# Kernel optimization log

Hardware: AMD Instinct MI355X
Metric: run time of the kernel (lower is better)

## Reference

```python
import jax, jax.numpy as jnp
import numpy as np

C = 256
NH = 8
G = 32  # groupnorm groups (min(32, C))
EPS = 1e-6


def setup_inputs() -> dict:
    key = jax.random.key(0)
    ks = jax.random.split(key, 7)
    B, D, H, W = 2, 16, 16, 16
    x = jax.random.normal(ks[0], (B, C, D, H, W), dtype=jnp.float32)
    gn_gamma = jnp.ones((C,), jnp.float32)
    gn_beta = jnp.zeros((C,), jnp.float32)
    s = 1.0 / np.sqrt(C)
    qkv_w = jax.random.normal(ks[1], (3 * C, C), jnp.float32) * s  # 1x1x1 conv weight
    qkv_b = jnp.zeros((3 * C,), jnp.float32)
    proj_w = jax.random.normal(ks[2], (C, C), jnp.float32) * s
    proj_b = jnp.zeros((C,), jnp.float32)
    return {"x": x, "gn_gamma": gn_gamma, "gn_beta": gn_beta,
            "qkv_w": qkv_w, "qkv_b": qkv_b, "proj_w": proj_w, "proj_b": proj_b}


def _group_norm(x, gamma, beta):
    # x: [B, C, S]
    B, Cc, S = x.shape
    xg = x.reshape(B, G, (Cc // G) * S)
    mu = xg.mean(axis=-1, keepdims=True)
    var = xg.var(axis=-1, keepdims=True)
    xg = (xg - mu) * jax.lax.rsqrt(var + EPS)
    x = xg.reshape(B, Cc, S)
    return x * gamma[None, :, None] + beta[None, :, None]


def reference(x, gn_gamma, gn_beta, qkv_w, qkv_b, proj_w, proj_b):
    B, Cc, D, H, W = x.shape
    S = D * H * W
    hd = Cc // NH
    xf = x.reshape(B, Cc, S)
    h = _group_norm(xf, gn_gamma, gn_beta)
    # 1x1x1 conv == channel matmul: [B, 3C, S]
    qkv = jnp.einsum('oc,bcs->bos', qkv_w, h) + qkv_b[None, :, None]
    # torch path: reshape(B,3C,S).permute(0,2,1).chunk -> q=channels[0:C]
    q, k, v = qkv[:, :Cc], qkv[:, Cc:2 * Cc], qkv[:, 2 * Cc:]
    # [B, C, S] -> [B, NH, S, hd]
    def to_heads(t):
        return t.reshape(B, NH, hd, S).transpose(0, 1, 3, 2)
    q, k, v = to_heads(q), to_heads(k), to_heads(v)
    scale = hd ** (-0.5)
    attn = jax.nn.softmax(jnp.einsum('bnqd,bnkd->bnqk', q, k) * scale, axis=-1)
    o = jnp.einsum('bnqk,bnkd->bnqd', attn, v)  # [B, NH, S, hd]
    o = o.transpose(0, 1, 3, 2).reshape(B, Cc, S)  # back to [B, C, S]
    o = jnp.einsum('oc,bcs->bos', proj_w, o) + proj_b[None, :, None]
    return x + o.reshape(B, Cc, D, H, W)
```

## Files before the change

### kernel.cpp

```cpp
#include <hip/hip_runtime.h>
#include <cstddef>

#define S_LEN 4096
#define C_DIM 256
#define NHEADS 8
#define HDIM 32

typedef __attribute__((ext_vector_type(8))) _Float16 half8;
typedef __attribute__((ext_vector_type(4))) _Float16 half4;
typedef __attribute__((ext_vector_type(2))) _Float16 h2t;
typedef __attribute__((ext_vector_type(2))) __fp16 fp16x2;
typedef __attribute__((ext_vector_type(4))) float floatx4;

#define SC2F ((float)(0.17677669529663687 * 1.4426950408889634))

__global__ __launch_bounds__(256) void prep_stats(
    const float* __restrict__ qkv_w, const float* __restrict__ proj_w,
    const float* __restrict__ qkv_b, const float* __restrict__ x,
    _Float16* __restrict__ wq, _Float16* __restrict__ wp,
    float* __restrict__ qbias, float* __restrict__ pstat)
{
  const int blk = blockIdx.x;
  const int tid = threadIdx.x;
  if (blk < 512) {
    __shared__ float red[2][4];
    const int gb = blk >> 3, e = blk & 7;
    const int g = gb & 31, b = gb >> 5;
    const float* xb = x + ((size_t)b * C_DIM + g * 8) * S_LEN + e * 4096;
    const float4* x4 = (const float4*)xb;
    float sum = 0.f, sumsq = 0.f;
    #pragma unroll
    for (int i = 0; i < 4; ++i) {
      float4 v = x4[tid + i * 256];
      sum += v.x + v.y + v.z + v.w;
      sumsq += v.x * v.x + v.y * v.y + v.z * v.z + v.w * v.w;
    }
    for (int off = 1; off < 64; off <<= 1) {
      sum += __shfl_xor(sum, off, 64);
      sumsq += __shfl_xor(sumsq, off, 64);
    }
    const int wv = tid >> 6, lane = tid & 63;
    if (lane == 0) { red[0][wv] = sum; red[1][wv] = sumsq; }
    __syncthreads();
    if (tid == 0) {
      pstat[(gb * 8 + e) * 2 + 0] = red[0][0] + red[0][1] + red[0][2] + red[0][3];
      pstat[(gb * 8 + e) * 2 + 1] = red[1][0] + red[1][1] + red[1][2] + red[1][3];
    }
  } else {
    int idx = (blk - 512) * 256 + tid;
    if (idx < 768 * 256) {
      float v = qkv_w[idx];
      if (idx < 256 * 256) v *= SC2F;
      wq[idx] = (_Float16)v;
    } else if (idx < 768 * 256 + 256 * 256) {
      int i = idx - 768 * 256;
      wp[i] = (_Float16)proj_w[i];
    } else if (idx < 768 * 256 + 256 * 256 + 768) {
      int i = idx - (768 * 256 + 256 * 256);
      float bv = qkv_b[i];
      if (i < 256) bv *= SC2F;
      qbias[i] = bv;
    }
  }
}

__global__ __launch_bounds__(256) void xnorm(
    const float* __restrict__ x, const float* __restrict__ gamma,
    const float* __restrict__ beta, const float* __restrict__ pstat,
    _Float16* __restrict__ xt)
{
  __shared__ _Float16 Lt[16][264];
  const int tid = threadIdx.x;
  const int b = blockIdx.y;
  const int s0 = blockIdx.x * 16;
  const int c = tid;
  const int gb = b * 32 + (c >> 3);
  float s = 0.f, sq = 0.f;
  #pragma unroll
  for (int e = 0; e < 8; ++e) {
    s  += pstat[(gb * 8 + e) * 2 + 0];
    sq += pstat[(gb * 8 + e) * 2 + 1];
  }
  const float mean = s * (1.f / 32768.f);
  const float rstd = rsqrtf(sq * (1.f / 32768.f) - mean * mean + 1e-6f);
  const float ga = gamma[c] * rstd, be = beta[c] - mean * ga;
  const float4* xa = (const float4*)(x + ((size_t)b * C_DIM + c) * S_LEN + s0);
  #pragma unroll
  for (int i = 0; i < 4; ++i) {
    float4 v = xa[i];
    Lt[i * 4 + 0][c] = (_Float16)(v.x * ga + be);
    Lt[i * 4 + 1][c] = (_Float16)(v.y * ga + be);
    Lt[i * 4 + 2][c] = (_Float16)(v.z * ga + be);
    Lt[i * 4 + 3][c] = (_Float16)(v.w * ga + be);
  }
  __syncthreads();
  const int sl = tid >> 4, cc = (tid & 15) * 16;
  _Float16* dst = xt + ((size_t)b * S_LEN + s0 + sl) * C_DIM + cc;
  const _Float16* src = &Lt[sl][cc];
  *(half8*)(dst + 0) = *(const half8*)(src + 0);
  *(half8*)(dst + 8) = *(const half8*)(src + 8);
}

__global__ __launch_bounds__(256) void qkv_gemm(
    const _Float16* __restrict__ W, const float* __restrict__ bias,
    const _Float16* __restrict__ xt,
    _Float16* __restrict__ qo, _Float16* __restrict__ ko_,
    _Float16* __restrict__ vo)
{
  __shared__ __align__(16) _Float16 Ld[256 * 72];
  const int tid = threadIdx.x;
  const int b = blockIdx.z;
  const int s0 = blockIdx.y * 64;

  {
    const int sl = tid >> 2, cc = (tid & 3) * 64;
    const _Float16* src = xt + ((size_t)b * S_LEN + s0 + sl) * C_DIM + cc;
    _Float16* dst = &Ld[sl * 264 + cc];
    #pragma unroll
    for (int j = 0; j < 8; ++j)
      *(half8*)(dst + j * 8) = *(const half8*)(src + j * 8);
  }
  __syncthreads();

  const int lane = tid & 63, wv = tid >> 6;
  const int m = lane & 15, quad = lane >> 4;
  const int mtb = blockIdx.x * 16 + wv * 4;
  const _Float16* wrow[4];
  #pragma unroll
  for (int j = 0; j < 4; ++j)
    wrow[j] = W + (size_t)((mtb + j) * 16 + m) * C_DIM + quad * 8;
  const _Float16* lp = &Ld[m * 264 + quad * 8];

  floatx4 acc[4][4];
  #pragma unroll
  for (int j = 0; j < 4; ++j)
    #pragma unroll
    for (int s = 0; s < 4; ++s) acc[j][s] = (floatx4){0.f,0.f,0.f,0.f};

  #pragma unroll 2
  for (int k0 = 0; k0 < C_DIM; k0 += 32) {
    half8 b0 = *(const half8*)(lp + k0);
    half8 b1 = *(const half8*)(lp + 16 * 264 + k0);
    half8 b2 = *(const half8*)(lp + 32 * 264 + k0);
    half8 b3 = *(const half8*)(lp + 48 * 264 + k0);
    #pragma unroll
    for (int j = 0; j < 4; ++j) {
      half8 a = *(const half8*)(wrow[j] + k0);
      acc[j][0] = __builtin_amdgcn_mfma_f32_16x16x32_f16(a, b0, acc[j][0], 0, 0, 0);
      acc[j][1] = __builtin_amdgcn_mfma_f32_16x16x32_f16(a, b1, acc[j][1], 0, 0, 0);
      acc[j][2] = __builtin_amdgcn_mfma_f32_16x16x32_f16(a, b2, acc[j][2], 0, 0, 0);
      acc[j][3] = __builtin_amdgcn_mfma_f32_16x16x32_f16(a, b3, acc[j][3], 0, 0, 0);
    }
  }

  if (blockIdx.x < 2) {
    #pragma unroll
    for (int j = 0; j < 4; ++j) {
      const int ob = (mtb + j) * 16 + quad * 4;
      const float bv0 = bias[ob], bv1 = bias[ob + 1],
                  bv2 = bias[ob + 2], bv3 = bias[ob + 3];
      _Float16* dst = (ob < 256) ? qo : ko_;
      const int oo = ob & 255, n = oo >> 5, d0 = oo & 31;
      #pragma unroll
      for (int sub = 0; sub < 4; ++sub) {
        int s = s0 + sub * 16 + m;
        half4 h = { (_Float16)(acc[j][sub][0] + bv0), (_Float16)(acc[j][sub][1] + bv1),
                    (_Float16)(acc[j][sub][2] + bv2), (_Float16)(acc[j][sub][3] + bv3) };
        *(half4*)(dst + (((size_t)b * NHEADS + n) * S_LEN + s) * HDIM + d0) = h;
      }
    }
  } else {
    __syncthreads();
    _Float16* VLd = Ld;
    #pragma unroll
    for (int j = 0; j < 4; ++j) {
      const int ob = (mtb + j) * 16 + quad * 4;
      const int lch = (wv * 4 + j) * 16 + quad * 4;
      const float bv0 = bias[ob], bv1 = bias[ob + 1],
                  bv2 = bias[ob + 2], bv3 = bias[ob + 3];
      #pragma unroll
      for (int sub = 0; sub < 4; ++sub) {
        int s = sub * 16 + m;
        VLd[(lch + 0) * 72 + s] = (_Float16)(acc[j][sub][0] + bv0);
        VLd[(lch + 1) * 72 + s] = (_Float16)(acc[j][sub][1] + bv1);
        VLd[(lch + 2) * 72 + s] = (_Float16)(acc[j][sub][2] + bv2);
        VLd[(lch + 3) * 72 + s] = (_Float16)(acc[j][sub][3] + bv3);
      }
    }
    __syncthreads();
    const int sh3 = tid & 7, chl = tid >> 3;
    #pragma unroll
    for (int p = 0; p < 8; ++p) {
      const int ch = p * 32 + chl;
      const int n = ch >> 5, d = ch & 31;
      _Float16* dst = vo + ((size_t)(b * NHEADS + n) * HDIM + d) * S_LEN + s0 + sh3 * 8;
      *(half8*)dst = *(const half8*)(VLd + ch * 72 + sh3 * 8);
    }
  }
}

__global__ __launch_bounds__(512) void attn_kernel(
    const _Float16* __restrict__ q, const _Float16* __restrict__ k,
    const _Float16* __restrict__ v, _Float16* __restrict__ po,
    float* __restrict__ pl)
{
  __shared__ __align__(16) _Float16 Kl[2][128 * 40];
  __shared__ __align__(16) _Float16 Vl[2][32 * 136];
  const int tid = threadIdx.x;
  const int lane = tid & 63, wv = tid >> 6;
  const int m = lane & 15, quad = lane >> 4;
  const int n = blockIdx.y, b = blockIdx.z;
  const int qc = blockIdx.x >> 1, kh = blockIdx.x & 1;
  const int q0 = qc * 256 + wv * 32;
  const int bh = b * NHEADS + n;

  const _Float16* qb = q + (size_t)bh * S_LEN * HDIM;
  const _Float16* kb = k + (size_t)bh * S_LEN * HDIM + (size_t)kh * 2048 * HDIM;
  const _Float16* vb = v + (size_t)bh * HDIM * S_LEN + (size_t)kh * 2048;

  half8 qfA = *(const half8*)(qb + (size_t)(q0 + m) * HDIM + quad * 8);
  half8 qfB = *(const half8*)(qb + (size_t)(q0 + 16 + m) * HDIM + quad * 8);

  const int krow = wv * 16 + (lane >> 2), kc = (lane & 3) * 8;
  const int vrow = wv * 4 + (lane >> 4), vc = (lane & 15) * 8;
  const _Float16* kg = kb + (size_t)krow * HDIM + kc;
  const _Float16* vg = vb + (size_t)vrow * S_LEN + vc;
  const int klds = krow * 40 + kc;
  const int vlds = vrow * 136 + vc;

  int4 kreg = *(const int4*)kg;
  int4 vreg = *(const int4*)vg;
  const _Float16* kgp = kg + 128 * HDIM;
  const _Float16* vgp = vg + 128;

  floatx4 oA0 = {0.f,0.f,0.f,0.f}, oA1 = oA0, oB0 = oA0, oB1 = oA0;
  float lA0 = 0.f, lA1 = 0.f, lB0 = 0.f, lB1 = 0.f;
  const fp16x2 one2 = { (__fp16)1.0f, (__fp16)1.0f };
  const floatx4 zz = {0.f,0.f,0.f,0.f};

  #pragma unroll 2
  for (int it = 0; it < 16; ++it) {
    const int bufi = it & 1;
    *(int4*)(&Kl[bufi][klds]) = kreg;
    *(int4*)(&Vl[bufi][vlds]) = vreg;
    kreg = *(const int4*)kgp; kgp += 128 * HDIM;
    vreg = *(const int4*)vgp; vgp += 128;
    __syncthreads();
    const _Float16* Kb = Kl[bufi];
    const _Float16* Vb = Vl[bufi];

    #pragma unroll
    for (int t = 0; t < 8; ++t) {
      const int tt = (t + wv) & 7;
      half8 kf  = *(const half8*)(Kb + (tt * 16 + m) * 40 + quad * 8);
      half4 vf0 = *(const half4*)(Vb + m * 136 + tt * 16 + quad * 4);
      half4 vf1 = *(const half4*)(Vb + (16 + m) * 136 + tt * 16 + quad * 4);
      __builtin_amdgcn_s_setprio(1);
      floatx4 sA = __builtin_amdgcn_mfma_f32_16x16x32_f16(kf, qfA, zz, 0, 0, 0);
      floatx4 sB = __builtin_amdgcn_mfma_f32_16x16x32_f16(kf, qfB, zz, 0, 0, 0);
      __builtin_amdgcn_s_setprio(0);
      float eA0 = __builtin_amdgcn_exp2f(sA[0]);
      float eA1 = __builtin_amdgcn_exp2f(sA[1]);
      float eA2 = __builtin_amdgcn_exp2f(sA[2]);
      float eA3 = __builtin_amdgcn_exp2f(sA[3]);
      float eB0 = __builtin_amdgcn_exp2f(sB[0]);
      float eB1 = __builtin_amdgcn_exp2f(sB[1]);
      float eB2 = __builtin_amdgcn_exp2f(sB[2]);
      float eB3 = __builtin_amdgcn_exp2f(sB[3]);
      half4 pA, pB;
      fp16x2 pAlo = __builtin_amdgcn_cvt_pkrtz(eA0, eA1);
      fp16x2 pAhi = __builtin_amdgcn_cvt_pkrtz(eA2, eA3);
      fp16x2 pBlo = __builtin_amdgcn_cvt_pkrtz(eB0, eB1);
      fp16x2 pBhi = __builtin_amdgcn_cvt_pkrtz(eB2, eB3);
      *(fp16x2*)&pA = pAlo; *((fp16x2*)&pA + 1) = pAhi;
      *(fp16x2*)&pB = pBlo; *((fp16x2*)&pB + 1) = pBhi;
      lA0 = __builtin_amdgcn_fdot2(pAlo, one2, lA0, false);
      lA1 = __builtin_amdgcn_fdot2(pAhi, one2, lA1, false);
      lB0 = __builtin_amdgcn_fdot2(pBlo, one2, lB0, false);
      lB1 = __builtin_amdgcn_fdot2(pBhi, one2, lB1, false);
      __builtin_amdgcn_s_setprio(1);
      oA0 = __builtin_amdgcn_mfma_f32_16x16x16f16(vf0, pA, oA0, 0, 0, 0);
      oA1 = __builtin_amdgcn_mfma_f32_16x16x16f16(vf1, pA, oA1, 0, 0, 0);
      oB0 = __builtin_amdgcn_mfma_f32_16x16x16f16(vf0, pB, oB0, 0, 0, 0);
      oB1 = __builtin_amdgcn_mfma_f32_16x16x16f16(vf1, pB, oB1, 0, 0, 0);
      __builtin_amdgcn_s_setprio(0);
    }
  }
  float lA = lA0 + lA1, lB = lB0 + lB1;
  lA += __shfl_xor(lA, 16, 64); lA += __shfl_xor(lA, 32, 64);
  lB += __shfl_xor(lB, 16, 64); lB += __shfl_xor(lB, 32, 64);
  _Float16* pobase = po + (size_t)kh * 2097152 + ((size_t)bh * S_LEN) * HDIM;
  {
    _Float16* poh = pobase + (size_t)(q0 + m) * HDIM;
    half4 h0 = { (_Float16)oA0[0], (_Float16)oA0[1], (_Float16)oA0[2], (_Float16)oA0[3] };
    half4 h1 = { (_Float16)oA1[0], (_Float16)oA1[1], (_Float16)oA1[2], (_Float16)oA1[3] };
    *(half4*)(poh + quad * 4) = h0;
    *(half4*)(poh + 16 + quad * 4) = h1;
    if (quad == 0) pl[(size_t)kh * 65536 + (size_t)bh * S_LEN + q0 + m] = lA;
  }
  {
    _Float16* poh = pobase + (size_t)(q0 + 16 + m) * HDIM;
    half4 h0 = { (_Float16)oB0[0], (_Float16)oB0[1], (_Float16)oB0[2], (_Float16)oB0[3] };
    half4 h1 = { (_Float16)oB1[0], (_Float16)oB1[1], (_Float16)oB1[2], (_Float16)oB1[3] };
    *(half4*)(poh + quad * 4) = h0;
    *(half4*)(poh + 16 + quad * 4) = h1;
    if (quad == 0) pl[(size_t)kh * 65536 + (size_t)bh * S_LEN + q0 + 16 + m] = lB;
  }
}

__global__ __launch_bounds__(256) void proj_gemm(
    const _Float16* __restrict__ W, const float* __restrict__ bias,
    const _Float16* __restrict__ po, const float* __restrict__ pl,
    const float* __restrict__ x, float* __restrict__ out)
{
  __shared__ float Linv[512];
  const int tid = threadIdx.x;
  const int lane = tid & 63, wv = tid >> 6;
  const int m = lane & 15, quad = lane >> 4;
  const int mtb = blockIdx.x * 8 + wv * 2;
  const int s0 = blockIdx.y * 64;
  const int b = blockIdx.z;

  {
    const int nn = tid >> 5, jj = (tid & 31) * 2;
    size_t base = (size_t)(b * NHEADS + nn) * S_LEN + s0 + jj;
    float a0 = pl[base]     + pl[65536 + base];
    float a1 = pl[base + 1] + pl[65536 + base + 1];
    Linv[nn * 64 + jj]     = 1.f / a0;
    Linv[nn * 64 + jj + 1] = 1.f / a1;
  }
  __syncthreads();

  const _Float16* wrow0 = W + (size_t)((mtb + 0) * 16 + m) * C_DIM + quad * 8;
  const _Float16* wrow1 = W + (size_t)((mtb + 1) * 16 + m) * C_DIM + quad * 8;
  floatx4 acc[2][4];
  #pragma unroll
  for (int j = 0; j < 2; ++j)
    #pragma unroll
    for (int s = 0; s < 4; ++s) acc[j][s] = (floatx4){0.f,0.f,0.f,0.f};

  #pragma unroll
  for (int k0 = 0; k0 < C_DIM; k0 += 32) {
    const int n = k0 >> 5;
    const int d0 = quad * 8;
    half8 bf[4];
    #pragma unroll
    for (int sub = 0; sub < 4; ++sub) {
      size_t idx = (((size_t)(b * NHEADS + n)) * S_LEN + s0 + sub * 16 + m) * HDIM + d0;
      half8 a = *(const half8*)(po + idx);
      half8 c = *(const half8*)(po + 2097152 + idx);
      _Float16 iv = (_Float16)Linv[n * 64 + sub * 16 + m];
      bf[sub] = (a + c) * iv;
    }
    half8 af0 = *(const half8*)(wrow0 + k0);
    half8 af1 = *(const half8*)(wrow1 + k0);
    #pragma unroll
    for (int sub = 0; sub < 4; ++sub) {
      acc[0][sub] = __builtin_amdgcn_mfma_f32_16x16x32_f16(af0, bf[sub], acc[0][sub], 0, 0, 0);
      acc[1][sub] = __builtin_amdgcn_mfma_f32_16x16x32_f16(af1, bf[sub], acc[1][sub], 0, 0, 0);
    }
  }
  #pragma unroll
  for (int j = 0; j < 2; ++j)
    #pragma unroll
    for (int sub = 0; sub < 4; ++sub) {
      int s = s0 + sub * 16 + m;
      #pragma unroll
      for (int r = 0; r < 4; ++r) {
        int c = (mtb + j) * 16 + quad * 4 + r;
        size_t idx = ((size_t)b * C_DIM + c) * S_LEN + s;
        out[idx] = x[idx] + acc[j][sub][r] + bias[c];
      }
    }
}

extern "C" void kernel_launch(void* const* d_in, const int* in_sizes, int n_in,
                              void* d_out, int out_size, void* d_ws, size_t ws_size,
                              hipStream_t stream) {
  const float* x        = (const float*)d_in[0];
  const float* gn_gamma = (const float*)d_in[1];
  const float* gn_beta  = (const float*)d_in[2];
  const float* qkv_w    = (const float*)d_in[3];
  const float* qkv_b    = (const float*)d_in[4];
  const float* proj_w   = (const float*)d_in[5];
  const float* proj_b   = (const float*)d_in[6];
  float* out = (float*)d_out;

  const size_t n1 = (size_t)2 * S_LEN * C_DIM;
  char* ws = (char*)d_ws;
  _Float16* qx  = (_Float16*)ws;
  _Float16* kx  = qx + n1;
  _Float16* vx  = kx + n1;
  _Float16* wq  = vx + n1;
  _Float16* wp  = wq + 768 * 256;
  float*    qbias = (float*)(wp + 256 * 256);
  float*    pstat = qbias + 768;
  _Float16* po  = (_Float16*)(pstat + 1024);
  float*    pl  = (float*)(po + 2 * n1);
  _Float16* xt  = (_Float16*)(pl + 2 * 65536);

  prep_stats<<<1539, 256, 0, stream>>>(qkv_w, proj_w, qkv_b, x, wq, wp, qbias, pstat);
  xnorm<<<dim3(256, 2), 256, 0, stream>>>(x, gn_gamma, gn_beta, pstat, xt);
  qkv_gemm<<<dim3(3, 64, 2), 256, 0, stream>>>(wq, qbias, xt, qx, kx, vx);
  attn_kernel<<<dim3(32, 8, 2), 512, 0, stream>>>(qx, kx, vx, po, pl);
  proj_gemm<<<dim3(2, 64, 2), 256, 0, stream>>>(wp, proj_b, po, pl, x, out);
}
```

Baseline: 144.0 us.

## Drop split-K attention, normalize in-kernel, and vectorize weight conversion

The attention kernel no longer splits the key range across two blocks. Each block now processes all 4096 keys and divides by the softmax denominator before writing one fp16 output. This removes the partial-output and partial-sum buffers and the merge step in the projection GEMM. The cost is half as many attention blocks (256 of 512 threads), which lowers occupancy and parallelism on a large GPU. Weight conversion in prep_stats now uses float4 loads with four elements per thread, which cuts its block count.

```diff
diff --git a/kernel.cpp b/kernel.cpp
--- a/kernel.cpp
+++ b/kernel.cpp
@@ -46,17 +46,22 @@
       pstat[(gb * 8 + e) * 2 + 0] = red[0][0] + red[0][1] + red[0][2] + red[0][3];
       pstat[(gb * 8 + e) * 2 + 1] = red[1][0] + red[1][1] + red[1][2] + red[1][3];
     }
+  } else if (blk < 704) {
+    const int i = (blk - 512) * 1024 + tid * 4;
+    float4 v = *(const float4*)(qkv_w + i);
+    const float sc = (i < 65536) ? SC2F : 1.f;
+    half4 h = { (_Float16)(v.x * sc), (_Float16)(v.y * sc),
+                (_Float16)(v.z * sc), (_Float16)(v.w * sc) };
+    *(half4*)(wq + i) = h;
+  } else if (blk < 768) {
+    const int i = (blk - 704) * 1024 + tid * 4;
+    float4 v = *(const float4*)(proj_w + i);
+    half4 h = { (_Float16)v.x, (_Float16)v.y, (_Float16)v.z, (_Float16)v.w };
+    *(half4*)(wp + i) = h;
   } else {
-    int idx = (blk - 512) * 256 + tid;
-    if (idx < 768 * 256) {
-      float v = qkv_w[idx];
-      if (idx < 256 * 256) v *= SC2F;
-      wq[idx] = (_Float16)v;
-    } else if (idx < 768 * 256 + 256 * 256) {
-      int i = idx - 768 * 256;
-      wp[i] = (_Float16)proj_w[i];
-    } else if (idx < 768 * 256 + 256 * 256 + 768) {
-      int i = idx - (768 * 256 + 256 * 256);
+    #pragma unroll
+    for (int j = 0; j < 3; ++j) {
+      const int i = tid + j * 256;
       float bv = qkv_b[i];
       if (i < 256) bv *= SC2F;
       qbias[i] = bv;
@@ -201,8 +206,7 @@
 
 __global__ __launch_bounds__(512) void attn_kernel(
     const _Float16* __restrict__ q, const _Float16* __restrict__ k,
-    const _Float16* __restrict__ v, _Float16* __restrict__ po,
-    float* __restrict__ pl)
+    const _Float16* __restrict__ v, _Float16* __restrict__ o)
 {
   __shared__ __align__(16) _Float16 Kl[2][128 * 40];
   __shared__ __align__(16) _Float16 Vl[2][32 * 136];
@@ -210,13 +214,13 @@
   const int lane = tid & 63, wv = tid >> 6;
   const int m = lane & 15, quad = lane >> 4;
   const int n = blockIdx.y, b = blockIdx.z;
-  const int qc = blockIdx.x >> 1, kh = blockIdx.x & 1;
+  const int qc = blockIdx.x;
   const int q0 = qc * 256 + wv * 32;
   const int bh = b * NHEADS + n;
 
   const _Float16* qb = q + (size_t)bh * S_LEN * HDIM;
-  const _Float16* kb = k + (size_t)bh * S_LEN * HDIM + (size_t)kh * 2048 * HDIM;
-  const _Float16* vb = v + (size_t)bh * HDIM * S_LEN + (size_t)kh * 2048;
+  const _Float16* kb = k + (size_t)bh * S_LEN * HDIM;
+  const _Float16* vb = v + (size_t)bh * HDIM * S_LEN;
 
   half8 qfA = *(const half8*)(qb + (size_t)(q0 + m) * HDIM + quad * 8);
   half8 qfB = *(const half8*)(qb + (size_t)(q0 + 16 + m) * HDIM + quad * 8);
@@ -239,7 +243,7 @@
   const floatx4 zz = {0.f,0.f,0.f,0.f};
 
   #pragma unroll 2
-  for (int it = 0; it < 16; ++it) {
+  for (int it = 0; it < 32; ++it) {
     const int bufi = it & 1;
     *(int4*)(&Kl[bufi][klds]) = kreg;
     *(int4*)(&Vl[bufi][vlds]) = vreg;
@@ -289,31 +293,33 @@
   float lA = lA0 + lA1, lB = lB0 + lB1;
   lA += __shfl_xor(lA, 16, 64); lA += __shfl_xor(lA, 32, 64);
   lB += __shfl_xor(lB, 16, 64); lB += __shfl_xor(lB, 32, 64);
-  _Float16* pobase = po + (size_t)kh * 2097152 + ((size_t)bh * S_LEN) * HDIM;
+  const float rA = 1.f / lA, rB = 1.f / lB;
+  _Float16* obase = o + ((size_t)bh * S_LEN) * HDIM;
   {
-    _Float16* poh = pobase + (size_t)(q0 + m) * HDIM;
-    half4 h0 = { (_Float16)oA0[0], (_Float16)oA0[1], (_Float16)oA0[2], (_Float16)oA0[3] };
-    half4 h1 = { (_Float16)oA1[0], (_Float16)oA1[1], (_Float16)oA1[2], (_Float16)oA1[3] };
-    *(half4*)(poh + quad * 4) = h0;
-    *(half4*)(poh + 16 + quad * 4) = h1;
-    if (quad == 0) pl[(size_t)kh * 65536 + (size_t)bh * S_LEN + q0 + m] = lA;
+    _Float16* oh = obase + (size_t)(q0 + m) * HDIM;
+    half4 h0 = { (_Float16)(oA0[0] * rA), (_Float16)(oA0[1] * rA),
+                 (_Float16)(oA0[2] * rA), (_Float16)(oA0[3] * rA) };
+    half4 h1 = { (_Float16)(oA1[0] * rA), (_Float16)(oA1[1] * rA),
+                 (_Float16)(oA1[2] * rA), (_Float16)(oA1[3] * rA) };
+    *(half4*)(oh + quad * 4) = h0;
+    *(half4*)(oh + 16 + quad * 4) = h1;
   }
   {
-    _Float16* poh = pobase + (size_t)(q0 + 16 + m) * HDIM;
-    half4 h0 = { (_Float16)oB0[0], (_Float16)oB0[1], (_Float16)oB0[2], (_Float16)oB0[3] };
-    half4 h1 = { (_Float16)oB1[0], (_Float16)oB1[1], (_Float16)oB1[2], (_Float16)oB1[3] };
-    *(half4*)(poh + quad * 4) = h0;
-    *(half4*)(poh + 16 + quad * 4) = h1;
-    if (quad == 0) pl[(size_t)kh * 65536 + (size_t)bh * S_LEN + q0 + 16 + m] = lB;
+    _Float16* oh = obase + (size_t)(q0 + 16 + m) * HDIM;
+    half4 h0 = { (_Float16)(oB0[0] * rB), (_Float16)(oB0[1] * rB),
+                 (_Float16)(oB0[2] * rB), (_Float16)(oB0[3] * rB) };
+    half4 h1 = { (_Float16)(oB1[0] * rB), (_Float16)(oB1[1] * rB),
+                 (_Float16)(oB1[2] * rB), (_Float16)(oB1[3] * rB) };
+    *(half4*)(oh + quad * 4) = h0;
+    *(half4*)(oh + 16 + quad * 4) = h1;
   }
 }
 
 __global__ __launch_bounds__(256) void proj_gemm(
     const _Float16* __restrict__ W, const float* __restrict__ bias,
-    const _Float16* __restrict__ po, const float* __restrict__ pl,
+    const _Float16* __restrict__ o,
     const float* __restrict__ x, float* __restrict__ out)
 {
-  __shared__ float Linv[512];
   const int tid = threadIdx.x;
   const int lane = tid & 63, wv = tid >> 6;
   const int m = lane & 15, quad = lane >> 4;
@@ -321,16 +327,6 @@
   const int s0 = blockIdx.y * 64;
   const int b = blockIdx.z;
 
-  {
-    const int nn = tid >> 5, jj = (tid & 31) * 2;
-    size_t base = (size_t)(b * NHEADS + nn) * S_LEN + s0 + jj;
-    float a0 = pl[base]     + pl[65536 + base];
-    float a1 = pl[base + 1] + pl[65536 + base + 1];
-    Linv[nn * 64 + jj]     = 1.f / a0;
-    Linv[nn * 64 + jj + 1] = 1.f / a1;
-  }
-  __syncthreads();
-
   const _Float16* wrow0 = W + (size_t)((mtb + 0) * 16 + m) * C_DIM + quad * 8;
   const _Float16* wrow1 = W + (size_t)((mtb + 1) * 16 + m) * C_DIM + quad * 8;
   floatx4 acc[2][4];
@@ -347,10 +343,7 @@
     #pragma unroll
     for (int sub = 0; sub < 4; ++sub) {
       size_t idx = (((size_t)(b * NHEADS + n)) * S_LEN + s0 + sub * 16 + m) * HDIM + d0;
-      half8 a = *(const half8*)(po + idx);
-      half8 c = *(const half8*)(po + 2097152 + idx);
-      _Float16 iv = (_Float16)Linv[n * 64 + sub * 16 + m];
-      bf[sub] = (a + c) * iv;
+      bf[sub] = *(const half8*)(o + idx);
     }
     half8 af0 = *(const half8*)(wrow0 + k0);
     half8 af1 = *(const half8*)(wrow1 + k0);
@@ -395,13 +388,12 @@
   _Float16* wp  = wq + 768 * 256;
   float*    qbias = (float*)(wp + 256 * 256);
   float*    pstat = qbias + 768;
-  _Float16* po  = (_Float16*)(pstat + 1024);
-  float*    pl  = (float*)(po + 2 * n1);
-  _Float16* xt  = (_Float16*)(pl + 2 * 65536);
-
-  prep_stats<<<1539, 256, 0, stream>>>(qkv_w, proj_w, qkv_b, x, wq, wp, qbias, pstat);
+  _Float16* ox  = (_Float16*)(pstat + 1024);
+  _Float16* xt  = ox + n1;
+
+  prep_stats<<<769, 256, 0, stream>>>(qkv_w, proj_w, qkv_b, x, wq, wp, qbias, pstat);
   xnorm<<<dim3(256, 2), 256, 0, stream>>>(x, gn_gamma, gn_beta, pstat, xt);
   qkv_gemm<<<dim3(3, 64, 2), 256, 0, stream>>>(wq, qbias, xt, qx, kx, vx);
-  attn_kernel<<<dim3(32, 8, 2), 512, 0, stream>>>(qx, kx, vx, po, pl);
-  proj_gemm<<<dim3(2, 64, 2), 256, 0, stream>>>(wp, proj_b, po, pl, x, out);
-}
+  attn_kernel<<<dim3(16, 8, 2), 512, 0, stream>>>(qx, kx, vx, ox);
+  proj_gemm<<<dim3(2, 64, 2), 256, 0, stream>>>(wp, proj_b, ox, x, out);
+}
```

Measured after the change: 144.3 us. About the same (+0.2%).
